# Kernel optimization log

Hardware: AMD Instinct MI355X
Metric: run time of the kernel (lower is better)

## Reference

```python
import jax, jax.numpy as jnp
import numpy as np

B, S, E, H = 8, 1024, 1024, 16
D = E // H  # 64
HALF = D // 2  # 32


def _apply_rope(t, freqs):
    # t: (B, S, H, D), freqs: (S, HALF)
    emb = jnp.concatenate([freqs, freqs], axis=-1)  # (S, D)
    cos = jnp.cos(emb)[None, :, None, :]  # (1, S, 1, D)
    sin = jnp.sin(emb)[None, :, None, :]
    t1, t2 = t[..., :D // 2], t[..., D // 2:]
    rot = jnp.concatenate([-t2, t1], axis=-1)
    return t * cos + rot * sin


def setup_inputs() -> dict:
    key = jax.random.key(0)
    ks = jax.random.split(key, 10)
    std = 1.0 / np.sqrt(E)
    return {
        "hidden_states": jax.random.normal(ks[0], (B, S, E), jnp.float32),
        "rotary_pos_emb": jax.random.uniform(ks[1], (S, HALF), jnp.float32) * 10.0,
        "wq": jax.random.normal(ks[2], (E, E), jnp.float32) * std,
        "bq": jnp.zeros((E,), jnp.float32),
        "wk": jax.random.normal(ks[3], (E, E), jnp.float32) * std,
        "bk": jnp.zeros((E,), jnp.float32),
        "wv": jax.random.normal(ks[4], (E, E), jnp.float32) * std,
        "bv": jnp.zeros((E,), jnp.float32),
        "wo": jax.random.normal(ks[5], (E, E), jnp.float32) * std,
        "bo": jnp.zeros((E,), jnp.float32),
    }


def reference(hidden_states, rotary_pos_emb, wq, bq, wk, bk, wv, bv, wo, bo):
    b, s, e = hidden_states.shape
    # QKV projections -> (B, S, H, D)
    q = (hidden_states @ wq + bq).reshape(b, s, H, D)
    k = (hidden_states @ wk + bk).reshape(b, s, H, D)
    v = (hidden_states @ wv + bv).reshape(b, s, H, D)
    # rotary embedding (computed in fp32, matching the torch code)
    q = _apply_rope(q.astype(jnp.float32), rotary_pos_emb).astype(hidden_states.dtype)
    k = _apply_rope(k.astype(jnp.float32), rotary_pos_emb).astype(hidden_states.dtype)
    scale = 1.0 / np.sqrt(D)
    # attention scores (B, H, Sq, Sk)
    scores = jnp.einsum("bqhd,bkhd->bhqk", q, k) * scale
    attn = jax.nn.softmax(scores, axis=-1)
    out = jnp.einsum("bhqk,bkhd->bqhd", attn, v).reshape(b, s, e)
    return out @ wo + bo
```

## Files before the change

### kernel.cpp

```cpp
#include <hip/hip_runtime.h>
#include <hip/hip_bf16.h>

typedef __hip_bfloat16 bf16;
typedef __attribute__((ext_vector_type(8))) short bfrag;
typedef __attribute__((ext_vector_type(4))) float f32x4;

#define MFMA(a, b, c) __builtin_amdgcn_mfma_f32_16x16x32_bf16((a), (b), (c), 0, 0, 0)

__device__ __forceinline__ void async16(const void* g, void* l) {
  __builtin_amdgcn_global_load_lds(
      (const __attribute__((address_space(1))) unsigned int*)g,
      (__attribute__((address_space(3))) unsigned int*)l, 16, 0, 0);
}

__device__ __forceinline__ bfrag ldfrag(const bf16* p) { return *(const bfrag*)p; }

__device__ __forceinline__ unsigned short f2b(float f) {
  return __hip_bfloat16_raw(__float2bfloat16(f)).x;
}
__device__ __forceinline__ float b2f(short u) {
  __hip_bfloat16_raw r; r.x = (unsigned short)u;
  return __bfloat162float(__hip_bfloat16(r));
}

__device__ __forceinline__ bfrag scale8(bfrag x) {
  bfrag y;
#pragma unroll
  for (int i = 0; i < 8; i++) y[i] = (short)f2b(b2f(x[i]) * 0.125f);
  return y;
}

__device__ __forceinline__ void pack4_store(bf16* p, f32x4 v, float s) {
  union { unsigned short h[4]; uint2 u; } pk;
#pragma unroll
  for (int i = 0; i < 4; i++) pk.h[i] = f2b(v[i] * s);
  *(uint2*)p = pk.u;
}


__global__ void k_convert_x(const float* __restrict__ X, unsigned short* __restrict__ Xb,
                            const float* __restrict__ rp, float* __restrict__ ctab,
                            float* __restrict__ stab) {
  int i = blockIdx.x * 256 + threadIdx.x;
  if (blockIdx.x < 128) {
    float f = rp[i];
    ctab[i] = cosf(f);
    stab[i] = sinf(f);
  }
  float4 v = *(const float4*)(X + (size_t)i * 4);
  union { unsigned short h[4]; uint2 u; } pk;
  pk.h[0] = f2b(v.x); pk.h[1] = f2b(v.y); pk.h[2] = f2b(v.z); pk.h[3] = f2b(v.w);
  *(uint2*)(Xb + (size_t)i * 4) = pk.u;
}

__global__ void k_transpose_w(const float* __restrict__ wq, const float* __restrict__ wk,
                              const float* __restrict__ wv, const float* __restrict__ wo,
                              unsigned short* __restrict__ tq, unsigned short* __restrict__ tk,
                              unsigned short* __restrict__ tv, unsigned short* __restrict__ to) {
  __shared__ unsigned short T[64][72];
  const int z = blockIdx.z;
  const float* src = (z == 0) ? wq : (z == 1) ? wk : (z == 2) ? wv : wo;
  unsigned short* dst = (z == 0) ? tq : (z == 1) ? tk : (z == 2) ? tv : to;
  const int k0 = blockIdx.y * 64, n0 = blockIdx.x * 64;
  const int t = threadIdx.x;
  const int kr = t >> 4;
  const int nc = (t & 15) * 4;
#pragma unroll
  for (int g = 0; g < 4; g++) {
    float4 v = *(const float4*)(src + (size_t)(k0 + g * 16 + kr) * 1024 + n0 + nc);
    const int kk = g * 16 + kr;
    T[nc + 0][kk] = f2b(v.x);
    T[nc + 1][kk] = f2b(v.y);
    T[nc + 2][kk] = f2b(v.z);
    T[nc + 3][kk] = f2b(v.w);
  }
  __syncthreads();
  const int nr = t >> 2;
  const int kc = (t & 3) * 16;
  unsigned short* dp = dst + (size_t)(n0 + nr) * 1024 + k0 + kc;
  *(uint4*)(dp + 0) = *(const uint4*)(&T[nr][kc + 0]);
  *(uint4*)(dp + 8) = *(const uint4*)(&T[nr][kc + 8]);
}


__device__ __forceinline__ void gemm128_rope(bf16* As, bf16* Bs, int m0, int n0,
                                             const bf16* __restrict__ A,
                                             const bf16* __restrict__ BT,
                                             const float* __restrict__ bias,
                                             bf16* __restrict__ C,
                                             const float* __restrict__ ctab,
                                             const float* __restrict__ stab) {
  const int tid = threadIdx.x;
  const int w = tid >> 6, l = tid & 63;
  const int wm = (w >> 1) << 6, wn = (w & 1) << 6;
  const int c = l & 15, quad = l >> 4;
  const int c7 = c & 7;

  f32x4 acc[4][4] = {};

  const int rl = l >> 3, ch = l & 7;
  const int sc = (ch ^ rl) * 8;
  const bf16* gA = A + (size_t)(m0 + w * 32 + rl) * 1024 + sc;
  const bf16* gB = BT + (size_t)(w * 32 + rl) * 1024 + sc;
  char* lA = (char*)As + w * 32 * 128;
  char* lB = (char*)Bs + w * 32 * 128;

  for (int k0 = 0; k0 < 1024; k0 += 64) {
    __syncthreads();
#pragma unroll
    for (int g = 0; g < 4; g++) {
      async16(gA + (size_t)g * 8 * 1024 + k0, lA + g * 1024);
      async16(gB + (size_t)g * 8 * 1024 + k0, lB + g * 1024);
    }
    __syncthreads();
#pragma unroll
    for (int ks = 0; ks < 2; ks++) {
      bfrag a[4], b[4];
#pragma unroll
      for (int i = 0; i < 4; i++)
        a[i] = ldfrag(&As[(wm + i * 16 + c) * 64 + (((ks * 4 + quad) ^ c7) * 8)]);
#pragma unroll
      for (int j = 0; j < 4; j++)
        b[j] = ldfrag(&Bs[(wn + j * 16 + c) * 64 + (((ks * 4 + quad) ^ c7) * 8)]);
#pragma unroll
      for (int i = 0; i < 4; i++)
#pragma unroll
        for (int j = 0; j < 4; j++) acc[i][j] = MFMA(a[i], b[j], acc[i][j]);
    }
  }

#pragma unroll
  for (int i = 0; i < 4; i++) {
    const int mb = m0 + wm + i * 16 + quad * 4;
#pragma unroll
    for (int j = 0; j < 2; j++) {
      const int n1 = n0 + wn + j * 16 + c;
      const int n2 = n1 + 32;
      const int dl = j * 16 + c;
      const float b1 = bias[n1];
      const float b2 = bias[n2];
#pragma unroll
      for (int r = 0; r < 4; r++) {
        const int m = mb + r;
        const int s = m & 1023;
        const float cs = ctab[s * 32 + dl];
        const float sn = stab[s * 32 + dl];
        const float t1 = acc[i][j][r] + b1;
        const float t2 = acc[i][j + 2][r] + b2;
        C[(size_t)m * 1024 + n1] = __float2bfloat16(t1 * cs - t2 * sn);
        C[(size_t)m * 1024 + n2] = __float2bfloat16(t2 * cs + t1 * sn);
      }
    }
  }
}

template <bool F32OUT, bool BIAS_ROW, int CSTRIDE>
__device__ __forceinline__ void gemm64_core(bf16* As, bf16* Bs, int m0, int n0,
                                            const bf16* __restrict__ A,
                                            const bf16* __restrict__ BT,
                                            const float* __restrict__ bias,
                                            bf16* __restrict__ C, float* __restrict__ Cf) {
  const int tid = threadIdx.x;
  const int w = tid >> 6, l = tid & 63;
  const int wm = (w >> 1) << 5, wn = (w & 1) << 6;
  const int c = l & 15, quad = l >> 4;
  const int c7 = c & 7;

  f32x4 acc[2][4] = {};

  const int rl = l >> 3, ch = l & 7;
  const int sc = (ch ^ rl) * 8;
  const bf16* gA = A + (size_t)(m0 + w * 16 + rl) * 1024 + sc;
  const bf16* gB = BT + (size_t)(w * 32 + rl) * 1024 + sc;
  char* lA = (char*)As + w * 16 * 128;
  char* lB = (char*)Bs + w * 32 * 128;

  for (int k0 = 0; k0 < 1024; k0 += 64) {
    __syncthreads();
#pragma unroll
    for (int g = 0; g < 2; g++) async16(gA + (size_t)g * 8 * 1024 + k0, lA + g * 1024);
#pragma unroll
    for (int g = 0; g < 4; g++) async16(gB + (size_t)g * 8 * 1024 + k0, lB + g * 1024);
    __syncthreads();
#pragma unroll
    for (int ks = 0; ks < 2; ks++) {
      bfrag a[2], b[4];
#pragma unroll
      for (int i = 0; i < 2; i++)
        a[i] = ldfrag(&As[(wm + i * 16 + c) * 64 + (((ks * 4 + quad) ^ c7) * 8)]);
#pragma unroll
      for (int j = 0; j < 4; j++)
        b[j] = ldfrag(&Bs[(wn + j * 16 + c) * 64 + (((ks * 4 + quad) ^ c7) * 8)]);
#pragma unroll
      for (int i = 0; i < 2; i++)
#pragma unroll
        for (int j = 0; j < 4; j++) acc[i][j] = MFMA(a[i], b[j], acc[i][j]);
    }
  }

#pragma unroll
  for (int i = 0; i < 2; i++) {
    const int mb = m0 + wm + i * 16 + quad * 4;
    float brow[4];
    if (BIAS_ROW) {
#pragma unroll
      for (int r = 0; r < 4; r++) brow[r] = bias[mb + r];
    }
#pragma unroll
    for (int j = 0; j < 4; j++) {
      const int n = n0 + wn + j * 16 + c;
      const float bcol = BIAS_ROW ? 0.0f : bias[n];
#pragma unroll
      for (int r = 0; r < 4; r++) {
        const float val = acc[i][j][r] + (BIAS_ROW ? brow[r] : bcol);
        if (F32OUT)
          Cf[(size_t)(mb + r) * CSTRIDE + n] = val;
        else
          C[(size_t)(mb + r) * CSTRIDE + n] = __float2bfloat16(val);
      }
    }
  }
}

__global__ __launch_bounds__(256) void k_gemm_qk(
    const bf16* __restrict__ X, const bf16* __restrict__ wqkT, const float* __restrict__ bq,
    const float* __restrict__ bk, const float* __restrict__ ctab,
    const float* __restrict__ stab, bf16* __restrict__ Q, bf16* __restrict__ Kb) {
  __shared__ __align__(16) bf16 As[128 * 64];
  __shared__ __align__(16) bf16 Bs[128 * 64];
  const int nblk = blockIdx.y;
  const bf16* BT = wqkT + (size_t)nblk * 128 * 1024;
  const bool isK = nblk >= 8;
  gemm128_rope(As, Bs, blockIdx.x * 128, (nblk & 7) * 128, X, BT, isK ? bk : bq,
               isK ? Kb : Q, ctab, stab);
}

__global__ __launch_bounds__(256) void k_gemm_vt(const bf16* __restrict__ wvT,
                                                 const bf16* __restrict__ X,
                                                 const float* __restrict__ bv,
                                                 bf16* __restrict__ VT) {
  __shared__ __align__(16) bf16 As[64 * 64];
  __shared__ __align__(16) bf16 Bs[128 * 64];
  gemm64_core<false, true, 8192>(As, Bs, blockIdx.y * 64, blockIdx.x * 128, wvT,
                                 X + (size_t)blockIdx.x * 128 * 1024, bv, VT, nullptr);
}

__global__ __launch_bounds__(256) void k_gemm_o(const bf16* __restrict__ A,
                                                const bf16* __restrict__ woT,
                                                const float* __restrict__ bias,
                                                float* __restrict__ Cf) {
  __shared__ __align__(16) bf16 As[64 * 64];
  __shared__ __align__(16) bf16 Bs[128 * 64];
  gemm64_core<true, false, 1024>(As, Bs, blockIdx.x * 64, blockIdx.y * 128, A,
                                 woT + (size_t)blockIdx.y * 128 * 1024, bias, nullptr, Cf);
}


__global__ __launch_bounds__(256, 4) void k_flash(const bf16* __restrict__ Q,
                                                  const bf16* __restrict__ K,
                                                  const bf16* __restrict__ VT,
                                                  bf16* __restrict__ O) {
  __shared__ __align__(16) bf16 Ks[64 * 64];
  __shared__ __align__(16) bf16 Vs[64 * 64];
  __shared__ __align__(16) bf16 Ps[4][32 * 72];
  const int qt = blockIdx.y, bh = blockIdx.x;
  const int b = bh >> 4, h = bh & 15;
  const int tid = threadIdx.x, w = tid >> 6, l = tid & 63;
  const int c = l & 15, quad = l >> 4;
  const int c7 = c & 7;

  bfrag qf[2][2];
#pragma unroll
  for (int qs = 0; qs < 2; qs++) {
    const bf16* qp =
        Q + (size_t)(b * 1024 + qt * 128 + w * 32 + qs * 16 + c) * 1024 + h * 64 + quad * 8;
    qf[qs][0] = scale8(ldfrag(qp));
    qf[qs][1] = scale8(ldfrag(qp + 32));
  }

  bfrag onesf;
#pragma unroll
  for (int i = 0; i < 8; i++) onesf[i] = (short)0x3F80;

  f32x4 oacc[2][4] = {};
  f32x4 lacc[2] = {};

  const int sr = l >> 3, scc = l & 7;
  const int swz = (scc ^ sr) * 8;
  const bf16* gK0 = K + (size_t)(b * 1024 + w * 16 + sr) * 1024 + h * 64 + swz;
  const bf16* gV0 = VT + (size_t)(h * 64 + w * 16 + sr) * 8192 + b * 1024 + swz;
  char* lK = (char*)Ks + w * 2048;
  char* lV = (char*)Vs + w * 2048;
  bf16* psw = Ps[w];

  for (int kt = 0; kt < 16; kt++) {
    __syncthreads();
    async16(gK0 + (size_t)(kt * 64) * 1024, lK);
    async16(gK0 + (size_t)(kt * 64 + 8) * 1024, lK + 1024);
    async16(gV0 + kt * 64, lV);
    async16(gV0 + 8 * 8192 + kt * 64, lV + 1024);
    __syncthreads();

#pragma unroll
    for (int qs = 0; qs < 2; qs++) {
      f32x4 sacc[4] = {};
#pragma unroll
      for (int mj = 0; mj < 4; mj++) {
        bfrag k0 = ldfrag(&Ks[(mj * 16 + c) * 64 + (quad ^ c7) * 8]);
        bfrag k1 = ldfrag(&Ks[(mj * 16 + c) * 64 + ((quad + 4) ^ c7) * 8]);
        sacc[mj] = MFMA(k0, qf[qs][0], sacc[mj]);
        sacc[mj] = MFMA(k1, qf[qs][1], sacc[mj]);
      }
      const int psrow = (qs * 16 + c) * 72;
#pragma unroll
      for (int mj = 0; mj < 4; mj++) {
        f32x4 p;
#pragma unroll
        for (int r = 0; r < 4; r++) p[r] = __expf(sacc[mj][r]);
        pack4_store(&psw[psrow + mj * 16 + quad * 4], p, 1.0f);
      }
    }

    bfrag pf[2][2];
#pragma unroll
    for (int qs = 0; qs < 2; qs++) {
      pf[qs][0] = ldfrag(&psw[(qs * 16 + c) * 72 + quad * 8]);
      pf[qs][1] = ldfrag(&psw[(qs * 16 + c) * 72 + 32 + quad * 8]);
      lacc[qs] = MFMA(onesf, pf[qs][0], lacc[qs]);
      lacc[qs] = MFMA(onesf, pf[qs][1], lacc[qs]);
    }
#pragma unroll
    for (int dj = 0; dj < 4; dj++) {
      bfrag v0 = ldfrag(&Vs[(dj * 16 + c) * 64 + (quad ^ c7) * 8]);
      bfrag v1 = ldfrag(&Vs[(dj * 16 + c) * 64 + ((quad + 4) ^ c7) * 8]);
#pragma unroll
      for (int qs = 0; qs < 2; qs++) {
        oacc[qs][dj] = MFMA(v0, pf[qs][0], oacc[qs][dj]);
        oacc[qs][dj] = MFMA(v1, pf[qs][1], oacc[qs][dj]);
      }
    }
  }

#pragma unroll
  for (int qs = 0; qs < 2; qs++) {
    const float inv = 1.0f / lacc[qs][0];
    bf16* op =
        O + (size_t)(b * 1024 + qt * 128 + w * 32 + qs * 16 + c) * 1024 + h * 64 + quad * 4;
#pragma unroll
    for (int dj = 0; dj < 4; dj++) pack4_store(op + dj * 16, oacc[qs][dj], inv);
  }
}


extern "C" void kernel_launch(void* const* d_in, const int* in_sizes, int n_in,
                              void* d_out, int out_size, void* d_ws, size_t ws_size,
                              hipStream_t stream) {
  const float* X  = (const float*)d_in[0];
  const float* rp = (const float*)d_in[1];
  const float* wq = (const float*)d_in[2];
  const float* bq = (const float*)d_in[3];
  const float* wk = (const float*)d_in[4];
  const float* bk = (const float*)d_in[5];
  const float* wv = (const float*)d_in[6];
  const float* bv = (const float*)d_in[7];
  const float* wo = (const float*)d_in[8];
  const float* bo = (const float*)d_in[9];
  float* out = (float*)d_out;

  char* ws = (char*)d_ws;
  const size_t MB = 1024 * 1024;
  bf16* Xb  = (bf16*)(ws + 0 * MB);
  bf16* Q   = (bf16*)(ws + 16 * MB);
  bf16* Kb  = (bf16*)(ws + 32 * MB);
  bf16* VT  = (bf16*)(ws + 48 * MB);
  bf16* O   = (bf16*)(ws + 64 * MB);
  bf16* wqT = (bf16*)(ws + 80 * MB);
  bf16* wkT = (bf16*)(ws + 82 * MB);
  bf16* wvT = (bf16*)(ws + 84 * MB);
  bf16* woT = (bf16*)(ws + 86 * MB);
  float* ctab = (float*)(ws + 88 * MB);
  float* stab = ctab + 1024 * 32;

  k_convert_x<<<dim3(8192), dim3(256), 0, stream>>>(X, (unsigned short*)Xb, rp, ctab, stab);
  k_transpose_w<<<dim3(16, 16, 4), dim3(256), 0, stream>>>(
      wq, wk, wv, wo, (unsigned short*)wqT, (unsigned short*)wkT, (unsigned short*)wvT,
      (unsigned short*)woT);
  k_gemm_qk<<<dim3(64, 16), dim3(256), 0, stream>>>(Xb, wqT, bq, bk, ctab, stab, Q, Kb);
  k_gemm_vt<<<dim3(64, 16), dim3(256), 0, stream>>>(wvT, Xb, bv, VT);
  k_flash<<<dim3(128, 8), dim3(256), 0, stream>>>(Q, Kb, VT, O);
  k_gemm_o<<<dim3(128, 8), dim3(256), 0, stream>>>(O, woT, bo, out);
}
```

Measured before the change: 238.0 us.

## Load K/V fragments directly from global memory in flash kernel, drop LDS staging

Result: slower. 319.7 us (+34.3%).

```diff
diff --git a/kernel.cpp b/kernel.cpp
--- a/kernel.cpp
+++ b/kernel.cpp
@@ -31,9 +31,11 @@
 }
 
 __device__ __forceinline__ void pack4_store(bf16* p, f32x4 v, float s) {
-  union { unsigned short h[4]; uint2 u; } pk;
-#pragma unroll
-  for (int i = 0; i < 4; i++) pk.h[i] = f2b(v[i] * s);
+  float2 lo; lo.x = v[0] * s; lo.y = v[1] * s;
+  float2 hi; hi.x = v[2] * s; hi.y = v[3] * s;
+  union { __hip_bfloat162 h2[2]; uint2 u; } pk;
+  pk.h2[0] = __float22bfloat162_rn(lo);
+  pk.h2[1] = __float22bfloat162_rn(hi);
   *(uint2*)p = pk.u;
 }
 
@@ -260,14 +262,11 @@
                                                   const bf16* __restrict__ K,
                                                   const bf16* __restrict__ VT,
                                                   bf16* __restrict__ O) {
-  __shared__ __align__(16) bf16 Ks[64 * 64];
-  __shared__ __align__(16) bf16 Vs[64 * 64];
   __shared__ __align__(16) bf16 Ps[4][32 * 72];
   const int qt = blockIdx.y, bh = blockIdx.x;
   const int b = bh >> 4, h = bh & 15;
   const int tid = threadIdx.x, w = tid >> 6, l = tid & 63;
   const int c = l & 15, quad = l >> 4;
-  const int c7 = c & 7;
 
   bfrag qf[2][2];
 #pragma unroll
@@ -285,31 +284,26 @@
   f32x4 oacc[2][4] = {};
   f32x4 lacc[2] = {};
 
-  const int sr = l >> 3, scc = l & 7;
-  const int swz = (scc ^ sr) * 8;
-  const bf16* gK0 = K + (size_t)(b * 1024 + w * 16 + sr) * 1024 + h * 64 + swz;
-  const bf16* gV0 = VT + (size_t)(h * 64 + w * 16 + sr) * 8192 + b * 1024 + swz;
-  char* lK = (char*)Ks + w * 2048;
-  char* lV = (char*)Vs + w * 2048;
+  const bf16* kb = K + (size_t)(b * 1024 + c) * 1024 + h * 64 + quad * 8;
+  const bf16* vb = VT + (size_t)(h * 64 + c) * 8192 + b * 1024 + quad * 8;
   bf16* psw = Ps[w];
 
   for (int kt = 0; kt < 16; kt++) {
-    __syncthreads();
-    async16(gK0 + (size_t)(kt * 64) * 1024, lK);
-    async16(gK0 + (size_t)(kt * 64 + 8) * 1024, lK + 1024);
-    async16(gV0 + kt * 64, lV);
-    async16(gV0 + 8 * 8192 + kt * 64, lV + 1024);
-    __syncthreads();
+    const bf16* kk = kb + (size_t)(kt * 64) * 1024;
+    bfrag kf[4][2];
+#pragma unroll
+    for (int mj = 0; mj < 4; mj++) {
+      kf[mj][0] = ldfrag(kk + (size_t)(mj * 16) * 1024);
+      kf[mj][1] = ldfrag(kk + (size_t)(mj * 16) * 1024 + 32);
+    }
 
 #pragma unroll
     for (int qs = 0; qs < 2; qs++) {
       f32x4 sacc[4] = {};
 #pragma unroll
       for (int mj = 0; mj < 4; mj++) {
-        bfrag k0 = ldfrag(&Ks[(mj * 16 + c) * 64 + (quad ^ c7) * 8]);
-        bfrag k1 = ldfrag(&Ks[(mj * 16 + c) * 64 + ((quad + 4) ^ c7) * 8]);
-        sacc[mj] = MFMA(k0, qf[qs][0], sacc[mj]);
-        sacc[mj] = MFMA(k1, qf[qs][1], sacc[mj]);
+        sacc[mj] = MFMA(kf[mj][0], qf[qs][0], sacc[mj]);
+        sacc[mj] = MFMA(kf[mj][1], qf[qs][1], sacc[mj]);
       }
       const int psrow = (qs * 16 + c) * 72;
 #pragma unroll
@@ -329,10 +323,12 @@
       lacc[qs] = MFMA(onesf, pf[qs][0], lacc[qs]);
       lacc[qs] = MFMA(onesf, pf[qs][1], lacc[qs]);
     }
+
+    const bf16* vv = vb + kt * 64;
 #pragma unroll
     for (int dj = 0; dj < 4; dj++) {
-      bfrag v0 = ldfrag(&Vs[(dj * 16 + c) * 64 + (quad ^ c7) * 8]);
-      bfrag v1 = ldfrag(&Vs[(dj * 16 + c) * 64 + ((quad + 4) ^ c7) * 8]);
+      bfrag v0 = ldfrag(vv + (size_t)(dj * 16) * 8192);
+      bfrag v1 = ldfrag(vv + (size_t)(dj * 16) * 8192 + 32);
 #pragma unroll
       for (int qs = 0; qs < 2; qs++) {
         oacc[qs][dj] = MFMA(v0, pf[qs][0], oacc[qs][dj]);
```
